# Kernel tuning notes

Measured on AMD Instinct MI355X. Metric: run time of the kernel, lower is better.

## Reference

```python
import jax, jax.numpy as jnp
import numpy as np

N, M, D_MODEL, H, D_K, D_V = 2048, 2048, 1024, 16, 64, 64


def setup_inputs() -> dict:
    key = jax.random.key(0)
    ks = jax.random.split(key, 12)
    s = D_MODEL ** -0.5
    Q = jax.random.normal(ks[0], (N, D_MODEL), dtype=jnp.float32)
    K = jax.random.normal(ks[1], (M, D_MODEL), dtype=jnp.float32)
    V = jax.random.normal(ks[2], (M, D_MODEL), dtype=jnp.float32)
    mask = jnp.ones((N, M), dtype=bool)  # unused by the original forward
    # stacked per-head Linear params (torch Linear: y = x @ W.T + b); here stored as (H, in, out)
    Wq = jax.random.normal(ks[3], (H, D_MODEL, D_K), dtype=jnp.float32) * s
    bq = jax.random.normal(ks[4], (H, D_K), dtype=jnp.float32) * 0.01
    Wk = jax.random.normal(ks[5], (H, D_MODEL, D_K), dtype=jnp.float32) * s
    bk = jax.random.normal(ks[6], (H, D_K), dtype=jnp.float32) * 0.01
    Wv = jax.random.normal(ks[7], (H, D_MODEL, D_V), dtype=jnp.float32) * s
    bv = jax.random.normal(ks[8], (H, D_V), dtype=jnp.float32) * 0.01
    Wo = jax.random.normal(ks[9], (H * D_V, D_MODEL), dtype=jnp.float32) * ((H * D_V) ** -0.5)
    bo = jax.random.normal(ks[10], (D_MODEL,), dtype=jnp.float32) * 0.01
    return dict(Q=Q, K=K, V=V, mask=mask, Wq=Wq, bq=bq, Wk=Wk, bk=bk,
                Wv=Wv, bv=bv, Wo=Wo, bo=bo)


def reference(Q, K, V, mask, Wq, bq, Wk, bk, Wv, bv, Wo, bo):
    # per-head projections, batched over heads (h)
    Qh = jnp.einsum('nd,hdk->hnk', Q, Wq) + bq[:, None, :]  # (H, n, d_k)
    Kh = jnp.einsum('md,hdk->hmk', K, Wk) + bk[:, None, :]  # (H, m, d_k)
    Vh = jnp.einsum('md,hdv->hmv', V, Wv) + bv[:, None, :]  # (H, m, d_v)
    # faithful to source: scale d_k**-0.5 is applied AFTER the softmax
    scores = jnp.einsum('hnk,hmk->hnm', Qh, Kh)             # (H, n, m)
    attn = jax.nn.softmax(scores, axis=-1) * (D_K ** -0.5)
    heads = jnp.einsum('hnm,hmv->hnv', attn, Vh)            # (H, n, d_v)
    concat = jnp.transpose(heads, (1, 0, 2)).reshape(heads.shape[1], H * D_V)
    return concat @ Wo + bo                                  # (n, d_model)
```

## Files before the change

### kernel.cpp

```cpp
#include <hip/hip_runtime.h>

#define N_TOK 2048
#define DMODEL 1024
#define NH 16
#define DK 64
#define SOFF 48.0f

typedef __attribute__((ext_vector_type(8))) short bfrag;
typedef __attribute__((ext_vector_type(4))) float f32x4;
typedef __attribute__((ext_vector_type(16))) float f32x16;
typedef __attribute__((ext_vector_type(4))) unsigned u32x4;

__device__ __forceinline__ unsigned short f2bf(float f) {
    unsigned u = __builtin_bit_cast(unsigned, f);
    u += 0x7FFFu + ((u >> 16) & 1u);
    return (unsigned short)(u >> 16);
}
__device__ __forceinline__ float bf2f(unsigned short u) {
    unsigned x = ((unsigned)u) << 16;
    return __builtin_bit_cast(float, x);
}
__device__ __forceinline__ unsigned cvtpk(float lo, float hi) {
    unsigned r;
    asm volatile("v_cvt_pk_bf16_f32 %0, %1, %2" : "=v"(r) : "v"(lo), "v"(hi));
    return r;
}

__device__ __forceinline__ int swz(int row, int b) {
    return row * 128 + (b ^ ((row & 7) << 4));
}

__device__ __forceinline__ void gload16(const void* g, void* l) {
    __builtin_amdgcn_global_load_lds(
        (__attribute__((address_space(1))) void*)g,
        (__attribute__((address_space(3))) void*)l,
        16, 0, 0);
}

__global__ __launch_bounds__(256) void prep_kernel(
    const float* __restrict__ Qin, const float* __restrict__ Kin, const float* __restrict__ Vin,
    const float* __restrict__ Wq_, const float* __restrict__ Wk_, const float* __restrict__ Wv_,
    const float* __restrict__ Wo_,
    unsigned short* __restrict__ AhQ, unsigned short* __restrict__ AhK, unsigned short* __restrict__ AhV,
    unsigned short* __restrict__ WthQ, unsigned short* __restrict__ WthK, unsigned short* __restrict__ WthV,
    unsigned short* __restrict__ WtlQ, unsigned short* __restrict__ WtlK,
    unsigned short* __restrict__ WoT)
{
    const int bid = blockIdx.x;
    const int tid = threadIdx.x;
    __shared__ float lds[64][65];

    if (bid < 3072) {
        const int z = bid >> 10, x = bid & 1023;
        const float* src = (z == 0) ? Qin : (z == 1) ? Kin : Vin;
        unsigned short* dh = (z == 0) ? AhQ : (z == 1) ? AhK : AhV;
        size_t base = ((size_t)x * 256 + tid) * 8;
        float4 a = *reinterpret_cast<const float4*>(src + base);
        float4 b = *reinterpret_cast<const float4*>(src + base + 4);
        float f[8] = {a.x, a.y, a.z, a.w, b.x, b.y, b.z, b.w};
        unsigned short hb[8];
        #pragma unroll
        for (int i = 0; i < 8; ++i) hb[i] = f2bf(f[i]);
        *reinterpret_cast<uint4*>(dh + base) = *reinterpret_cast<const uint4*>(hb);
    } else if (bid < 3840) {
        const int t = bid - 3072;
        const int z = t >> 8, rem = t & 255;
        const int h = rem >> 4, dt = rem & 15;
        const float* W = (z == 0) ? Wq_ : (z == 1) ? Wk_ : Wv_;
        unsigned short* oh = (z == 0) ? WthQ : (z == 1) ? WthK : WthV;
        unsigned short* ol = (z == 0) ? WtlQ : WtlK;

        {
            int rr = tid >> 2, c4 = (tid & 3) * 16;
            const float* src = W + ((size_t)h * DMODEL + dt * 64 + rr) * DK + c4;
            #pragma unroll
            for (int i = 0; i < 4; ++i) {
                float4 v = *reinterpret_cast<const float4*>(src + i * 4);
                lds[rr][c4 + i * 4 + 0] = v.x;
                lds[rr][c4 + i * 4 + 1] = v.y;
                lds[rr][c4 + i * 4 + 2] = v.z;
                lds[rr][c4 + i * 4 + 3] = v.w;
            }
        }
        __syncthreads();
        {
            int kk_ = tid >> 2, d4 = (tid & 3) * 16;
            unsigned short hb[16], lb[16];
            #pragma unroll
            for (int i = 0; i < 16; ++i) {
                float v = lds[d4 + i][kk_];
                hb[i] = f2bf(v);
                lb[i] = f2bf(v - bf2f(hb[i]));
            }
            size_t o = (size_t)(h * 64 + kk_) * DMODEL + dt * 64 + d4;
            *reinterpret_cast<uint4*>(oh + o)     = *reinterpret_cast<const uint4*>(hb);
            *reinterpret_cast<uint4*>(oh + o + 8) = *reinterpret_cast<const uint4*>(hb + 8);
            if (z < 2) {
                *reinterpret_cast<uint4*>(ol + o)     = *reinterpret_cast<const uint4*>(lb);
                *reinterpret_cast<uint4*>(ol + o + 8) = *reinterpret_cast<const uint4*>(lb + 8);
            }
        }
    } else {
        const int t = bid - 3840;
        const int dt = t >> 4, jt = t & 15;
        {
            int rr = tid >> 2, c4 = (tid & 3) * 16;
            const float* src = Wo_ + (size_t)(dt * 64 + rr) * DMODEL + jt * 64 + c4;
            #pragma unroll
            for (int i = 0; i < 4; ++i) {
                float4 v = *reinterpret_cast<const float4*>(src + i * 4);
                lds[rr][c4 + i * 4 + 0] = v.x;
                lds[rr][c4 + i * 4 + 1] = v.y;
                lds[rr][c4 + i * 4 + 2] = v.z;
                lds[rr][c4 + i * 4 + 3] = v.w;
            }
        }
        __syncthreads();
        {
            int jj = tid >> 2, d4 = (tid & 3) * 16;
            unsigned short hb[16];
            #pragma unroll
            for (int i = 0; i < 16; ++i) hb[i] = f2bf(lds[d4 + i][jj]);
            size_t o = (size_t)(jt * 64 + jj) * DMODEL + dt * 64 + d4;
            *reinterpret_cast<uint4*>(WoT + o)     = *reinterpret_cast<const uint4*>(hb);
            *reinterpret_cast<uint4*>(WoT + o + 8) = *reinterpret_cast<const uint4*>(hb + 8);
        }
    }
}

__global__ __launch_bounds__(256) void proj_kernel(
    const unsigned short* __restrict__ AhQ, const unsigned short* __restrict__ AhK, const unsigned short* __restrict__ AhV,
    const unsigned short* __restrict__ WthQ, const unsigned short* __restrict__ WthK, const unsigned short* __restrict__ WthV,
    const unsigned short* __restrict__ WtlQ, const unsigned short* __restrict__ WtlK,
    const float* __restrict__ bq_, const float* __restrict__ bk_, const float* __restrict__ bv_,
    unsigned short* __restrict__ Qhh,
    unsigned short* __restrict__ Khh,
    unsigned short* __restrict__ Vt)
{
    const int z = blockIdx.z;
    const unsigned short* Ah = (z == 0) ? AhK : (z == 1) ? AhQ : AhV;
    const unsigned short* Bh = (z == 0) ? WthK : (z == 1) ? WthQ : WthV;
    const unsigned short* Bl = (z == 0) ? WtlK : WtlQ;
    const float* bias = (z == 0) ? bk_ : (z == 1) ? bq_ : bv_;

    __shared__ alignas(16) unsigned char sAh[16384];
    __shared__ alignas(16) unsigned char sBh[16384];
    __shared__ alignas(16) unsigned char sBl[16384];

    const int tid = threadIdx.x;
    const int lane = tid & 63;
    const int w = tid >> 6;
    const int wm = w >> 1, wn = w & 1;
    const int g = lane >> 4, li = lane & 15;

    const int row0 = blockIdx.x * 128;
    const int col0 = blockIdx.y * 128;

    f32x4 acc[4][4];
    #pragma unroll
    for (int m = 0; m < 4; ++m)
        #pragma unroll
        for (int n = 0; n < 4; ++n) acc[m][n] = f32x4{0.f, 0.f, 0.f, 0.f};

    for (int kt = 0; kt < DMODEL; kt += 64) {
        __syncthreads();
        #pragma unroll
        for (int p = 0; p < 4; ++p) {
            int chunk = p * 256 + tid;
            int r = chunk >> 3, cc = chunk & 7;
            int cs = (cc * 8) ^ ((r & 7) << 3);
            int ldso = (p * 256 + w * 64) * 16;
            gload16(Ah + (size_t)(row0 + r) * DMODEL + kt + cs, sAh + ldso);
            gload16(Bh + (size_t)(col0 + r) * DMODEL + kt + cs, sBh + ldso);
            if (z < 2)
                gload16(Bl + (size_t)(col0 + r) * DMODEL + kt + cs, sBl + ldso);
        }
        __syncthreads();

        if (z < 2) {
            #pragma unroll
            for (int kk = 0; kk < 2; ++kk) {
                bfrag afh[4], bfh[4], bfl[4];
                #pragma unroll
                for (int m = 0; m < 4; ++m)
                    afh[m] = *reinterpret_cast<const bfrag*>(sAh + swz(wm * 64 + m * 16 + li, kk * 64 + g * 16));
                #pragma unroll
                for (int n = 0; n < 4; ++n) {
                    bfh[n] = *reinterpret_cast<const bfrag*>(sBh + swz(wn * 64 + n * 16 + li, kk * 64 + g * 16));
                    bfl[n] = *reinterpret_cast<const bfrag*>(sBl + swz(wn * 64 + n * 16 + li, kk * 64 + g * 16));
                }
                #pragma unroll
                for (int m = 0; m < 4; ++m)
                    #pragma unroll
                    for (int n = 0; n < 4; ++n) {
                        acc[m][n] = __builtin_amdgcn_mfma_f32_16x16x32_bf16(afh[m], bfh[n], acc[m][n], 0, 0, 0);
                        acc[m][n] = __builtin_amdgcn_mfma_f32_16x16x32_bf16(afh[m], bfl[n], acc[m][n], 0, 0, 0);
                    }
            }
        } else {
            #pragma unroll
            for (int kk = 0; kk < 2; ++kk) {
                bfrag afh[4], bfh[4];
                #pragma unroll
                for (int m = 0; m < 4; ++m)
                    afh[m] = *reinterpret_cast<const bfrag*>(sAh + swz(wm * 64 + m * 16 + li, kk * 64 + g * 16));
                #pragma unroll
                for (int n = 0; n < 4; ++n)
                    bfh[n] = *reinterpret_cast<const bfrag*>(sBh + swz(wn * 64 + n * 16 + li, kk * 64 + g * 16));
                #pragma unroll
                for (int m = 0; m < 4; ++m)
                    #pragma unroll
                    for (int n = 0; n < 4; ++n)
                        acc[m][n] = __builtin_amdgcn_mfma_f32_16x16x32_bf16(afh[m], bfh[n], acc[m][n], 0, 0, 0);
            }
        }
    }

    #pragma unroll
    for (int m = 0; m < 4; ++m) {
        #pragma unroll
        for (int n = 0; n < 4; ++n) {
            int colg = col0 + wn * 64 + n * 16 + li;
            float bb = bias[colg];
            int hh = colg >> 6, k = colg & 63;
            int rowb = row0 + wm * 64 + m * 16 + g * 4;
            if (z == 2) {
                unsigned short vb4[4];
                #pragma unroll
                for (int r = 0; r < 4; ++r) vb4[r] = f2bf(acc[m][n][r] + bb);
                *reinterpret_cast<uint2*>(Vt + ((size_t)hh * DK + k) * N_TOK + rowb) =
                    *reinterpret_cast<const uint2*>(vb4);
            } else {
                #pragma unroll
                for (int r = 0; r < 4; ++r) {
                    size_t o = ((size_t)hh * N_TOK + rowb + r) * DK + k;
                    float val = acc[m][n][r] + bb;
                    if (z == 1) val *= 1.44269504088896f;
                    if (z == 0) Khh[o] = f2bf(val);
                    else        Qhh[o] = f2bf(val);
                }
            }
        }
    }
}

__global__ __launch_bounds__(256) void attn_kernel(
    const unsigned short* __restrict__ Qhh,
    const unsigned short* __restrict__ Khh,
    const unsigned short* __restrict__ Vt,
    unsigned short* __restrict__ Opart, float* __restrict__ lbuf)
{
    __shared__ alignas(16) unsigned char sKh[3][8192];
    __shared__ alignas(16) unsigned char sV [3][8192];

    const int bid = blockIdx.x;
    const int orig = (bid & 7) * 128 + (bid >> 3);
    const int h       = orig >> 6;
    const int quarter = (orig >> 4) & 3;
    const int qt      = orig & 15;

    const int tid  = threadIdx.x;
    const int lane = tid & 63;
    const int w    = tid >> 6;
    const int q31  = lane & 31;
    const int hi   = lane >> 5;
    const int qrow0 = qt * 128 + w * 32;

    const unsigned short* QbH = Qhh + (size_t)h * N_TOK * DK;
    const unsigned short* KbH = Khh + (size_t)h * N_TOK * DK;
    const unsigned short* Vtb = Vt  + (size_t)h * DK * N_TOK;

    bfrag bqh[4];
    #pragma unroll
    for (int d = 0; d < 4; ++d)
        bqh[d] = *reinterpret_cast<const bfrag*>(
            QbH + (size_t)(qrow0 + q31) * DK + d * 16 + hi * 8);

    f32x16 acc0 = {}, acc1 = {};
    float lrun = 0.f;

    const int tbase = quarter * (N_TOK / 4);

#define STAGE(B, T) do {                                                     \
    _Pragma("unroll")                                                        \
    for (int p_ = 0; p_ < 2; ++p_) {                                         \
        int chunk_ = p_ * 256 + w * 64 + lane;                               \
        int r_ = chunk_ >> 3;                                                \
        int cs_ = ((chunk_ & 7) * 8) ^ ((r_ & 7) << 3);                      \
        int ldso_ = (p_ * 256 + w * 64) * 16;                                \
        gload16(KbH + (size_t)((T) + r_) * DK + cs_, sKh[B] + ldso_);        \
        gload16(Vtb + (size_t)r_ * N_TOK + (T) + cs_, sV[B] + ldso_);        \
    } } while (0)

#define MKFRAG(W, PF) do {                                                   \
    _Pragma("unroll")                                                        \
    for (int kk_ = 0; kk_ < 2; ++kk_) {                                      \
        unsigned b0_ = W[4 * kk_ + 0], b1_ = W[4 * kk_ + 1];                 \
        unsigned a0_ = W[4 * kk_ + 2], a1_ = W[4 * kk_ + 3];                 \
        unsigned sb0_ = (unsigned)__shfl_xor((int)b0_, 32);                  \
        unsigned sa0_ = (unsigned)__shfl_xor((int)a0_, 32);                  \
        unsigned sb1_ = (unsigned)__shfl_xor((int)b1_, 32);                  \
        unsigned sa1_ = (unsigned)__shfl_xor((int)a1_, 32);                  \
        u32x4 t_ = { hi ? sa0_ : b0_, hi ? sa1_ : b1_,                       \
                     hi ? a0_ : sb0_, hi ? a1_ : sb1_ };                     \
        PF[kk_] = __builtin_bit_cast(bfrag, t_);                             \
    } } while (0)

    STAGE(0, tbase);

    int cur = 0;
    for (int tt = 0; tt < 8; ++tt) {
        int nxt = cur + 1; if (nxt == 3) nxt = 0;
        if (tt < 7) {
            STAGE(nxt, tbase + (tt + 1) * 64);
            asm volatile("s_waitcnt vmcnt(4)" ::: "memory");
        } else {
            asm volatile("s_waitcnt vmcnt(0)" ::: "memory");
        }
        __builtin_amdgcn_s_barrier();
        asm volatile("" ::: "memory");

        f32x16 s0, s1;
        #pragma unroll
        for (int r = 0; r < 16; ++r) { s0[r] = -SOFF; s1[r] = -SOFF; }
        __builtin_amdgcn_s_setprio(1);
        #pragma unroll
        for (int d = 0; d < 4; ++d) {
            const int bo = d * 32 + hi * 16;
            bfrag kh0 = *reinterpret_cast<const bfrag*>(sKh[cur] + swz(q31,      bo));
            bfrag kh1 = *reinterpret_cast<const bfrag*>(sKh[cur] + swz(32 + q31, bo));
            s0 = __builtin_amdgcn_mfma_f32_32x32x16_bf16(kh0, bqh[d], s0, 0, 0, 0);
            s1 = __builtin_amdgcn_mfma_f32_32x32x16_bf16(kh1, bqh[d], s1, 0, 0, 0);
        }
        __builtin_amdgcn_s_setprio(0);

        float p0[16], p1[16];
        #pragma unroll
        for (int r = 0; r < 16; ++r) p0[r] = __builtin_exp2f(s0[r]);
        #pragma unroll
        for (int r = 0; r < 16; ++r) p1[r] = __builtin_exp2f(s1[r]);
        float ps = ((p0[0] + p0[1]) + (p0[2] + p0[3])) + ((p0[4] + p0[5]) + (p0[6] + p0[7]))
                 + ((p0[8] + p0[9]) + (p0[10] + p0[11])) + ((p0[12] + p0[13]) + (p0[14] + p0[15]))
                 + ((p1[0] + p1[1]) + (p1[2] + p1[3])) + ((p1[4] + p1[5]) + (p1[6] + p1[7]))
                 + ((p1[8] + p1[9]) + (p1[10] + p1[11])) + ((p1[12] + p1[13]) + (p1[14] + p1[15]));
        ps += __shfl_xor(ps, 32);
        lrun += ps;

        unsigned w0[8], w1[8];
        #pragma unroll
        for (int j = 0; j < 8; ++j) w0[j] = cvtpk(p0[2 * j], p0[2 * j + 1]);
        #pragma unroll
        for (int j = 0; j < 8; ++j) w1[j] = cvtpk(p1[2 * j], p1[2 * j + 1]);
        bfrag pf0[2], pf1[2];
        MKFRAG(w0, pf0);
        MKFRAG(w1, pf1);

        __builtin_amdgcn_s_setprio(1);
        #pragma unroll
        for (int ks = 0; ks < 4; ++ks) {
            bfrag pb = (ks < 2) ? pf0[ks & 1] : pf1[ks & 1];
            const int bo = ks * 32 + hi * 16;
            bfrag va0 = *reinterpret_cast<const bfrag*>(sV[cur] + swz(q31,      bo));
            bfrag va1 = *reinterpret_cast<const bfrag*>(sV[cur] + swz(32 + q31, bo));
            acc0 = __builtin_amdgcn_mfma_f32_32x32x16_bf16(va0, pb, acc0, 0, 0, 0);
            acc1 = __builtin_amdgcn_mfma_f32_32x32x16_bf16(va1, pb, acc1, 0, 0, 0);
        }
        __builtin_amdgcn_s_setprio(0);
        asm volatile("" ::: "memory");
        cur = nxt;
    }
#undef STAGE
#undef MKFRAG

    const size_t idxp = (size_t)quarter * NH * N_TOK + (size_t)h * N_TOK + qrow0 + q31;
    unsigned short* op = Opart + idxp * 64;
    #pragma unroll
    for (int m = 0; m < 4; ++m) {
        uint2 wa = make_uint2(cvtpk(acc0[4 * m], acc0[4 * m + 1]),
                              cvtpk(acc0[4 * m + 2], acc0[4 * m + 3]));
        uint2 wb = make_uint2(cvtpk(acc1[4 * m], acc1[4 * m + 1]),
                              cvtpk(acc1[4 * m + 2], acc1[4 * m + 3]));
        *reinterpret_cast<uint2*>(op + 8 * m + 4 * hi)      = wa;
        *reinterpret_cast<uint2*>(op + 32 + 8 * m + 4 * hi) = wb;
    }
    if (lane < 32)
        lbuf[idxp] = lrun;
}

__global__ __launch_bounds__(256) void combine_kernel(
    const unsigned short* __restrict__ Opart, const float* __restrict__ lbuf,
    unsigned short* __restrict__ Hc)
{
    const int tid = threadIdx.x;
    const int sub = tid & 3;
    const int idx = blockIdx.x * 64 + (tid >> 2);
    const int h = idx >> 11, row = idx & 2047;
    const int QS = NH * N_TOK;

    float lsum = 0.f;
    #pragma unroll
    for (int q = 0; q < 4; ++q) lsum += lbuf[(size_t)q * QS + idx];
    float inv = 0.125f / lsum;

    float acc[16];
    #pragma unroll
    for (int i = 0; i < 16; ++i) acc[i] = 0.f;
    #pragma unroll
    for (int q = 0; q < 4; ++q) {
        const unsigned short* Oq = Opart + ((size_t)q * QS + idx) * 64 + sub * 16;
        uint4 x = *reinterpret_cast<const uint4*>(Oq);
        uint4 y = *reinterpret_cast<const uint4*>(Oq + 8);
        unsigned wds[8] = {x.x, x.y, x.z, x.w, y.x, y.y, y.z, y.w};
        #pragma unroll
        for (int j = 0; j < 8; ++j) {
            acc[2 * j]     += bf2f((unsigned short)(wds[j] & 0xFFFF));
            acc[2 * j + 1] += bf2f((unsigned short)(wds[j] >> 16));
        }
    }
    unsigned short hb[16];
    #pragma unroll
    for (int i = 0; i < 16; ++i) hb[i] = f2bf(acc[i] * inv);
    size_t o = (size_t)row * DMODEL + h * 64 + sub * 16;
    *reinterpret_cast<uint4*>(Hc + o)     = *reinterpret_cast<const uint4*>(hb);
    *reinterpret_cast<uint4*>(Hc + o + 8) = *reinterpret_cast<const uint4*>(hb + 8);
}

__global__ __launch_bounds__(256) void oproj_kernel(
    const unsigned short* __restrict__ Hc,
    const unsigned short* __restrict__ WoT,
    const float* __restrict__ bo,
    float* __restrict__ out)
{
    __shared__ alignas(16) unsigned char sA[8192];
    __shared__ alignas(16) unsigned char sB[16384];

    const int tid = threadIdx.x;
    const int lane = tid & 63;
    const int w = tid >> 6;
    const int wm = w >> 1, wn = w & 1;
    const int g = lane >> 4, li = lane & 15;
    const int row0 = blockIdx.x * 64;
    const int col0 = blockIdx.y * 128;

    f32x4 acc[2][4];
    #pragma unroll
    for (int m = 0; m < 2; ++m)
        #pragma unroll
        for (int n = 0; n < 4; ++n) acc[m][n] = f32x4{0.f, 0.f, 0.f, 0.f};

    for (int kt = 0; kt < DMODEL; kt += 64) {
        __syncthreads();
        #pragma unroll
        for (int p = 0; p < 2; ++p) {
            int chunk = p * 256 + tid;
            int r = chunk >> 3, cc = chunk & 7;
            int cs = (cc * 8) ^ ((r & 7) << 3);
            int ldso = (p * 256 + w * 64) * 16;
            gload16(Hc + (size_t)(row0 + r) * DMODEL + kt + cs, sA + ldso);
        }
        #pragma unroll
        for (int p = 0; p < 4; ++p) {
            int chunk = p * 256 + tid;
            int r = chunk >> 3, cc = chunk & 7;
            int cs = (cc * 8) ^ ((r & 7) << 3);
            int ldso = (p * 256 + w * 64) * 16;
            gload16(WoT + (size_t)(col0 + r) * DMODEL + kt + cs, sB + ldso);
        }
        __syncthreads();

        #pragma unroll
        for (int kk = 0; kk < 2; ++kk) {
            bfrag af[2], bf_[4];
            #pragma unroll
            for (int m = 0; m < 2; ++m)
                af[m] = *reinterpret_cast<const bfrag*>(sA + swz(wm * 32 + m * 16 + li, kk * 64 + g * 16));
            #pragma unroll
            for (int n = 0; n < 4; ++n)
                bf_[n] = *reinterpret_cast<const bfrag*>(sB + swz(wn * 64 + n * 16 + li, kk * 64 + g * 16));
            #pragma unroll
            for (int m = 0; m < 2; ++m)
                #pragma unroll
                for (int n = 0; n < 4; ++n)
                    acc[m][n] = __builtin_amdgcn_mfma_f32_16x16x32_bf16(af[m], bf_[n], acc[m][n], 0, 0, 0);
        }
    }

    #pragma unroll
    for (int m = 0; m < 2; ++m) {
        #pragma unroll
        for (int n = 0; n < 4; ++n) {
            int colg = col0 + wn * 64 + n * 16 + li;
            float bb = bo[colg];
            #pragma unroll
            for (int r = 0; r < 4; ++r) {
                int rowg = row0 + wm * 32 + m * 16 + g * 4 + r;
                out[(size_t)rowg * DMODEL + colg] = acc[m][n][r] + bb;
            }
        }
    }
}

extern "C" void kernel_launch(void* const* d_in, const int* in_sizes, int n_in,
                              void* d_out, int out_size, void* d_ws, size_t ws_size,
                              hipStream_t stream) {
    (void)in_sizes; (void)n_in; (void)out_size; (void)ws_size;
    const float* Q  = (const float*)d_in[0];
    const float* K  = (const float*)d_in[1];
    const float* V  = (const float*)d_in[2];
    const float* Wq = (const float*)d_in[4];
    const float* bq = (const float*)d_in[5];
    const float* Wk = (const float*)d_in[6];
    const float* bk = (const float*)d_in[7];
    const float* Wv = (const float*)d_in[8];
    const float* bv = (const float*)d_in[9];
    const float* Wo = (const float*)d_in[10];
    const float* bo = (const float*)d_in[11];
    float* out = (float*)d_out;

    const size_t ASZ = (size_t)N_TOK * DMODEL;
    const size_t WSZ = (size_t)NH * DK * DMODEL;
    const size_t HSZ = (size_t)NH * N_TOK * DK;
    unsigned short* p = (unsigned short*)d_ws;
    unsigned short* AhQ = p; p += ASZ;
    unsigned short* AhK = p; p += ASZ;
    unsigned short* AhV = p; p += ASZ;
    unsigned short* WthQ = p; p += WSZ;
    unsigned short* WthK = p; p += WSZ;
    unsigned short* WthV = p; p += WSZ;
    unsigned short* WtlQ = p; p += WSZ;
    unsigned short* WtlK = p; p += WSZ;
    unsigned short* Qhh = p; p += HSZ;
    unsigned short* Khh = p; p += HSZ;
    unsigned short* Vt  = p; p += HSZ;
    unsigned short* Hc  = p; p += HSZ;
    unsigned short* WoT = p; p += ASZ / 2;

    unsigned short* Opart = (unsigned short*)d_ws;
    float* lbuf = (float*)(Opart + (size_t)4 * NH * N_TOK * 64);

    prep_kernel<<<dim3(4096), 256, 0, stream>>>(
        Q, K, V, Wq, Wk, Wv, Wo,
        AhQ, AhK, AhV, WthQ, WthK, WthV, WtlQ, WtlK, WoT);
    proj_kernel<<<dim3(16, 8, 3), 256, 0, stream>>>(
        AhQ, AhK, AhV, WthQ, WthK, WthV, WtlQ, WtlK,
        bq, bk, bv, Qhh, Khh, Vt);
    attn_kernel<<<dim3(1024), 256, 0, stream>>>(Qhh, Khh, Vt, Opart, lbuf);
    combine_kernel<<<dim3(512), 256, 0, stream>>>(Opart, lbuf, Hc);
    oproj_kernel<<<dim3(32, 8), 256, 0, stream>>>(Hc, WoT, bo, out);
}
```

Baseline: 105.8 us.

## Software-pipeline QK^T one tile ahead and drop Q low-part weight split

The attention loop moves from a 3-stage to a 4-stage LDS ring, prefetches two tiles ahead, and computes the next tile's QK^T MFMAs before the current tile's exp/PV work so matrix and vector work can overlap. Separately, the Q projection no longer uses the hi/lo bf16 split of the weights; only K keeps the extra-precision low part. This removes one weight buffer, its prep writes and the extra loads and MFMAs in the Q projection, at the cost of lower precision in Q and more registers and LDS in the attention kernel.

```diff
diff --git a/kernel.cpp b/kernel.cpp
--- a/kernel.cpp
+++ b/kernel.cpp
@@ -43,7 +43,7 @@
     const float* __restrict__ Wo_,
     unsigned short* __restrict__ AhQ, unsigned short* __restrict__ AhK, unsigned short* __restrict__ AhV,
     unsigned short* __restrict__ WthQ, unsigned short* __restrict__ WthK, unsigned short* __restrict__ WthV,
-    unsigned short* __restrict__ WtlQ, unsigned short* __restrict__ WtlK,
+    unsigned short* __restrict__ WtlK,
     unsigned short* __restrict__ WoT)
 {
     const int bid = blockIdx.x;
@@ -68,7 +68,6 @@
         const int h = rem >> 4, dt = rem & 15;
         const float* W = (z == 0) ? Wq_ : (z == 1) ? Wk_ : Wv_;
         unsigned short* oh = (z == 0) ? WthQ : (z == 1) ? WthK : WthV;
-        unsigned short* ol = (z == 0) ? WtlQ : WtlK;
 
         {
             int rr = tid >> 2, c4 = (tid & 3) * 16;
@@ -95,9 +94,9 @@
             size_t o = (size_t)(h * 64 + kk_) * DMODEL + dt * 64 + d4;
             *reinterpret_cast<uint4*>(oh + o)     = *reinterpret_cast<const uint4*>(hb);
             *reinterpret_cast<uint4*>(oh + o + 8) = *reinterpret_cast<const uint4*>(hb + 8);
-            if (z < 2) {
-                *reinterpret_cast<uint4*>(ol + o)     = *reinterpret_cast<const uint4*>(lb);
-                *reinterpret_cast<uint4*>(ol + o + 8) = *reinterpret_cast<const uint4*>(lb + 8);
+            if (z == 1) {
+                *reinterpret_cast<uint4*>(WtlK + o)     = *reinterpret_cast<const uint4*>(lb);
+                *reinterpret_cast<uint4*>(WtlK + o + 8) = *reinterpret_cast<const uint4*>(lb + 8);
             }
         }
     } else {
@@ -131,7 +130,7 @@
 __global__ __launch_bounds__(256) void proj_kernel(
     const unsigned short* __restrict__ AhQ, const unsigned short* __restrict__ AhK, const unsigned short* __restrict__ AhV,
     const unsigned short* __restrict__ WthQ, const unsigned short* __restrict__ WthK, const unsigned short* __restrict__ WthV,
-    const unsigned short* __restrict__ WtlQ, const unsigned short* __restrict__ WtlK,
+    const unsigned short* __restrict__ WtlK,
     const float* __restrict__ bq_, const float* __restrict__ bk_, const float* __restrict__ bv_,
     unsigned short* __restrict__ Qhh,
     unsigned short* __restrict__ Khh,
@@ -140,7 +139,6 @@
     const int z = blockIdx.z;
     const unsigned short* Ah = (z == 0) ? AhK : (z == 1) ? AhQ : AhV;
     const unsigned short* Bh = (z == 0) ? WthK : (z == 1) ? WthQ : WthV;
-    const unsigned short* Bl = (z == 0) ? WtlK : WtlQ;
     const float* bias = (z == 0) ? bk_ : (z == 1) ? bq_ : bv_;
 
     __shared__ alignas(16) unsigned char sAh[16384];
@@ -172,12 +170,12 @@
             int ldso = (p * 256 + w * 64) * 16;
             gload16(Ah + (size_t)(row0 + r) * DMODEL + kt + cs, sAh + ldso);
             gload16(Bh + (size_t)(col0 + r) * DMODEL + kt + cs, sBh + ldso);
-            if (z < 2)
-                gload16(Bl + (size_t)(col0 + r) * DMODEL + kt + cs, sBl + ldso);
+            if (z == 0)
+                gload16(WtlK + (size_t)(col0 + r) * DMODEL + kt + cs, sBl + ldso);
         }
         __syncthreads();
 
-        if (z < 2) {
+        if (z == 0) {
             #pragma unroll
             for (int kk = 0; kk < 2; ++kk) {
                 bfrag afh[4], bfh[4], bfl[4];
@@ -250,8 +248,8 @@
     const unsigned short* __restrict__ Vt,
     unsigned short* __restrict__ Opart, float* __restrict__ lbuf)
 {
-    __shared__ alignas(16) unsigned char sKh[3][8192];
-    __shared__ alignas(16) unsigned char sV [3][8192];
+    __shared__ alignas(16) unsigned char sKh[4][8192];
+    __shared__ alignas(16) unsigned char sV [4][8192];
 
     const int bid = blockIdx.x;
     const int orig = (bid & 7) * 128 + (bid >> 3);
@@ -291,6 +289,20 @@
         gload16(KbH + (size_t)((T) + r_) * DK + cs_, sKh[B] + ldso_);        \
         gload16(Vtb + (size_t)r_ * N_TOK + (T) + cs_, sV[B] + ldso_);        \
     } } while (0)
+
+#define QKT(B, S0, S1) do {                                                  \
+    _Pragma("unroll")                                                        \
+    for (int r_ = 0; r_ < 16; ++r_) { S0[r_] = -SOFF; S1[r_] = -SOFF; }      \
+    __builtin_amdgcn_s_setprio(1);                                           \
+    _Pragma("unroll")                                                        \
+    for (int d_ = 0; d_ < 4; ++d_) {                                         \
+        const int bo_ = d_ * 32 + hi * 16;                                   \
+        bfrag kh0_ = *reinterpret_cast<const bfrag*>(sKh[B] + swz(q31,      bo_)); \
+        bfrag kh1_ = *reinterpret_cast<const bfrag*>(sKh[B] + swz(32 + q31, bo_)); \
+        S0 = __builtin_amdgcn_mfma_f32_32x32x16_bf16(kh0_, bqh[d_], S0, 0, 0, 0);  \
+        S1 = __builtin_amdgcn_mfma_f32_32x32x16_bf16(kh1_, bqh[d_], S1, 0, 0, 0);  \
+    }                                                                        \
+    __builtin_amdgcn_s_setprio(0); } while (0)
 
 #define MKFRAG(W, PF) do {                                                   \
     _Pragma("unroll")                                                        \
@@ -307,12 +319,17 @@
     } } while (0)
 
     STAGE(0, tbase);
-
-    int cur = 0;
+    STAGE(1, tbase + 64);
+    asm volatile("s_waitcnt vmcnt(4)" ::: "memory");
+    __builtin_amdgcn_s_barrier();
+    asm volatile("" ::: "memory");
+
+    f32x16 s0c, s1c;
+    QKT(0, s0c, s1c);
+
     for (int tt = 0; tt < 8; ++tt) {
-        int nxt = cur + 1; if (nxt == 3) nxt = 0;
-        if (tt < 7) {
-            STAGE(nxt, tbase + (tt + 1) * 64);
+        if (tt < 6) {
+            STAGE((tt + 2) & 3, tbase + (tt + 2) * 64);
             asm volatile("s_waitcnt vmcnt(4)" ::: "memory");
         } else {
             asm volatile("s_waitcnt vmcnt(0)" ::: "memory");
@@ -320,25 +337,16 @@
         __builtin_amdgcn_s_barrier();
         asm volatile("" ::: "memory");
 
-        f32x16 s0, s1;
-        #pragma unroll
-        for (int r = 0; r < 16; ++r) { s0[r] = -SOFF; s1[r] = -SOFF; }
-        __builtin_amdgcn_s_setprio(1);
-        #pragma unroll
-        for (int d = 0; d < 4; ++d) {
-            const int bo = d * 32 + hi * 16;
-            bfrag kh0 = *reinterpret_cast<const bfrag*>(sKh[cur] + swz(q31,      bo));
-            bfrag kh1 = *reinterpret_cast<const bfrag*>(sKh[cur] + swz(32 + q31, bo));
-            s0 = __builtin_amdgcn_mfma_f32_32x32x16_bf16(kh0, bqh[d], s0, 0, 0, 0);
-            s1 = __builtin_amdgcn_mfma_f32_32x32x16_bf16(kh1, bqh[d], s1, 0, 0, 0);
-        }
-        __builtin_amdgcn_s_setprio(0);
+        f32x16 s0n, s1n;
+        if (tt < 7) {
+            QKT((tt + 1) & 3, s0n, s1n);
+        }
 
         float p0[16], p1[16];
         #pragma unroll
-        for (int r = 0; r < 16; ++r) p0[r] = __builtin_exp2f(s0[r]);
-        #pragma unroll
-        for (int r = 0; r < 16; ++r) p1[r] = __builtin_exp2f(s1[r]);
+        for (int r = 0; r < 16; ++r) p0[r] = __builtin_exp2f(s0c[r]);
+        #pragma unroll
+        for (int r = 0; r < 16; ++r) p1[r] = __builtin_exp2f(s1c[r]);
         float ps = ((p0[0] + p0[1]) + (p0[2] + p0[3])) + ((p0[4] + p0[5]) + (p0[6] + p0[7]))
                  + ((p0[8] + p0[9]) + (p0[10] + p0[11])) + ((p0[12] + p0[13]) + (p0[14] + p0[15]))
                  + ((p1[0] + p1[1]) + (p1[2] + p1[3])) + ((p1[4] + p1[5]) + (p1[6] + p1[7]))
@@ -360,16 +368,19 @@
         for (int ks = 0; ks < 4; ++ks) {
             bfrag pb = (ks < 2) ? pf0[ks & 1] : pf1[ks & 1];
             const int bo = ks * 32 + hi * 16;
-            bfrag va0 = *reinterpret_cast<const bfrag*>(sV[cur] + swz(q31,      bo));
-            bfrag va1 = *reinterpret_cast<const bfrag*>(sV[cur] + swz(32 + q31, bo));
+            bfrag va0 = *reinterpret_cast<const bfrag*>(sV[tt & 3] + swz(q31,      bo));
+            bfrag va1 = *reinterpret_cast<const bfrag*>(sV[tt & 3] + swz(32 + q31, bo));
             acc0 = __builtin_amdgcn_mfma_f32_32x32x16_bf16(va0, pb, acc0, 0, 0, 0);
             acc1 = __builtin_amdgcn_mfma_f32_32x32x16_bf16(va1, pb, acc1, 0, 0, 0);
         }
         __builtin_amdgcn_s_setprio(0);
         asm volatile("" ::: "memory");
-        cur = nxt;
+
+        s0c = s0n;
+        s1c = s1n;
     }
 #undef STAGE
+#undef QKT
 #undef MKFRAG
 
     const size_t idxp = (size_t)quarter * NH * N_TOK + (size_t)h * N_TOK + qrow0 + q31;
@@ -527,7 +538,6 @@
     unsigned short* WthQ = p; p += WSZ;
     unsigned short* WthK = p; p += WSZ;
     unsigned short* WthV = p; p += WSZ;
-    unsigned short* WtlQ = p; p += WSZ;
     unsigned short* WtlK = p; p += WSZ;
     unsigned short* Qhh = p; p += HSZ;
     unsigned short* Khh = p; p += HSZ;
@@ -540,9 +550,9 @@
 
     prep_kernel<<<dim3(4096), 256, 0, stream>>>(
         Q, K, V, Wq, Wk, Wv, Wo,
-        AhQ, AhK, AhV, WthQ, WthK, WthV, WtlQ, WtlK, WoT);
+        AhQ, AhK, AhV, WthQ, WthK, WthV, WtlK, WoT);
     proj_kernel<<<dim3(16, 8, 3), 256, 0, stream>>>(
-        AhQ, AhK, AhV, WthQ, WthK, WthV, WtlQ, WtlK,
+        AhQ, AhK, AhV, WthQ, WthK, WthV, WtlK,
         bq, bk, bv, Qhh, Khh, Vt);
     attn_kernel<<<dim3(1024), 256, 0, stream>>>(Qhh, Khh, Vt, Opart, lbuf);
     combine_kernel<<<dim3(512), 256, 0, stream>>>(Opart, lbuf, Hc);
```

After: 106.8 us. Within noise of the previous version (+0.9%).
